# Performance work log

Hardware: AMD Instinct MI355X
Metric: run time of the kernel (lower is better)

Reference implementation:

```python
import jax, jax.numpy as jnp
import numpy as np


def setup_inputs() -> dict:
    key = jax.random.key(0)
    ks = jax.random.split(key, 7)
    BSZ, L, V, D = 4096, 50, 100000, 256
    acts_request = jax.random.randint(ks[0], (BSZ, L), 0, V, dtype=jnp.int32)
    acts_slot = jax.random.randint(ks[1], (BSZ, L), 0, V, dtype=jnp.int32)
    acts_value = jax.random.randint(ks[2], (BSZ, L), 0, V, dtype=jnp.int32)
    slot_names = jax.random.randint(ks[3], (BSZ, 4), 0, V, dtype=jnp.int32)
    ontology_emb = jax.random.normal(ks[4], (V, D), dtype=jnp.float32)
    # torch.nn.init.uniform(-0.01, 0.01)
    w1 = jax.random.uniform(ks[5], (D, D), dtype=jnp.float32, minval=-0.01, maxval=0.01)
    w2 = jax.random.uniform(ks[6], (D, D), dtype=jnp.float32, minval=-0.01, maxval=0.01)
    return {"acts_request": acts_request, "acts_slot": acts_slot,
            "acts_value": acts_value, "slot_names": slot_names,
            "ontology_emb": ontology_emb, "w1": w1, "w2": w2}


def reference(acts_request, acts_slot, acts_value, slot_names, ontology_emb, w1, w2):
    # ragged embedding gather + sum over the act lists -> (bsz, d)
    t_q = ontology_emb[acts_request].sum(axis=1)
    t_s = ontology_emb[acts_slot].sum(axis=1)
    t_v = ontology_emb[acts_value].sum(axis=1)
    c_s = ontology_emb[slot_names]                      # (bsz, 4, d)
    # matmul(w1, t_q) per batch: (bsz, d)
    g_q = jnp.einsum('ij,bj->bi', w1, t_q)
    g_sv = jnp.einsum('ij,bj->bi', w2, t_s + t_v)
    gates = (c_s
             + jax.nn.sigmoid(c_s * g_q[:, None, :])
             + jax.nn.sigmoid(c_s * g_sv[:, None, :]))
    return gates  # (bsz, 4, d)
```

## Files before the change

### kernel.cpp

```cpp
#include <hip/hip_runtime.h>

#define BLK     256
#define TBATCH  4
#define LLEN    50
#define DIM     256
#define DIM4    64

__device__ __forceinline__ float sigmoidf_(float x) {
    return 1.0f / (1.0f + __expf(-x));
}

__global__ __launch_bounds__(256) void transpose_w(
    const float* __restrict__ w1, const float* __restrict__ w2,
    float* __restrict__ wt1, float* __restrict__ wt2)
{
    __shared__ float tile[64][65];
    const int m  = blockIdx.x >> 4;
    const int t  = blockIdx.x & 15;
    const int ti = (t >> 2) * 64;
    const int tj = (t & 3) * 64;
    const float* src = m ? w2  : w1;
    float*       dst = m ? wt2 : wt1;
    const int tx = threadIdx.x & 63;
    const int ty = threadIdx.x >> 6;
    #pragma unroll
    for (int r = 0; r < 64; r += 4) {
        const int row = r + ty;
        tile[row][tx] = src[(ti + row) * DIM + tj + tx];
    }
    __syncthreads();
    #pragma unroll
    for (int r = 0; r < 64; r += 4) {
        const int row = r + ty;
        dst[(tj + row) * DIM + ti + tx] = tile[tx][row];
    }
}

__global__ __launch_bounds__(BLK, 4) void slotgate_fused(
    const int* __restrict__ acts_request,
    const int* __restrict__ acts_slot,
    const int* __restrict__ acts_value,
    const int* __restrict__ slot_names,
    const float* __restrict__ emb,
    const float* __restrict__ wt1,
    const float* __restrict__ wt2,
    float* __restrict__ out)
{
    __shared__ int    lds_iq[TBATCH * LLEN];
    __shared__ int    lds_is[TBATCH * LLEN];
    __shared__ int    lds_iv[TBATCH * LLEN];
    __shared__ float4 lds_tq [TBATCH * DIM4];
    __shared__ float4 lds_tsv[TBATCH * DIM4];
    __shared__ float  lds_gq [TBATCH * DIM];
    __shared__ float  lds_gsv[TBATCH * DIM];

    const int tid  = threadIdx.x;
    const int b0   = blockIdx.x * TBATCH;
    const int wv   = tid >> 6;
    const int lane = tid & 63;

    for (int t = tid; t < TBATCH * LLEN; t += BLK) {
        lds_iq[t] = acts_request[b0 * LLEN + t];
        lds_is[t] = acts_slot   [b0 * LLEN + t];
        lds_iv[t] = acts_value  [b0 * LLEN + t];
    }
    __syncthreads();

    const float4* emb4 = (const float4*)emb;

    {
        float4 aq  = make_float4(0.f, 0.f, 0.f, 0.f);
        float4 asv = make_float4(0.f, 0.f, 0.f, 0.f);
        const int* iqp = &lds_iq[wv * LLEN];
        const int* isp = &lds_is[wv * LLEN];
        const int* ivp = &lds_iv[wv * LLEN];
        #pragma unroll 5
        for (int l = 0; l < LLEN; l++) {
            float4 vq = emb4[iqp[l] * DIM4 + lane];
            float4 vs = emb4[isp[l] * DIM4 + lane];
            float4 vv = emb4[ivp[l] * DIM4 + lane];
            aq.x  += vq.x;        aq.y  += vq.y;        aq.z  += vq.z;        aq.w  += vq.w;
            asv.x += vs.x + vv.x; asv.y += vs.y + vv.y; asv.z += vs.z + vv.z; asv.w += vs.w + vv.w;
        }
        lds_tq [wv * DIM4 + lane] = aq;
        lds_tsv[wv * DIM4 + lane] = asv;
    }
    __syncthreads();

    {
        const int i = wv * 64 + lane;
        float accq [TBATCH] = {};
        float accsv[TBATCH] = {};
        for (int j4 = 0; j4 < DIM4; j4++) {
            float tqa[TBATCH][4], tsa[TBATCH][4];
            #pragma unroll
            for (int r = 0; r < TBATCH; r++) {
                float4 v = lds_tq [r * DIM4 + j4];
                tqa[r][0] = v.x; tqa[r][1] = v.y; tqa[r][2] = v.z; tqa[r][3] = v.w;
                float4 u = lds_tsv[r * DIM4 + j4];
                tsa[r][0] = u.x; tsa[r][1] = u.y; tsa[r][2] = u.z; tsa[r][3] = u.w;
            }
            #pragma unroll
            for (int k = 0; k < 4; k++) {
                const int j = j4 * 4 + k;
                const float w1v = wt1[j * DIM + i];
                const float w2v = wt2[j * DIM + i];
                #pragma unroll
                for (int r = 0; r < TBATCH; r++) {
                    accq [r] += w1v * tqa[r][k];
                    accsv[r] += w2v * tsa[r][k];
                }
            }
        }
        #pragma unroll
        for (int r = 0; r < TBATCH; r++) {
            lds_gq [r * DIM + i] = accq [r];
            lds_gsv[r * DIM + i] = accsv[r];
        }
    }
    __syncthreads();

    {
        const int tb   = tid >> 6;
        const int tcol = tid & 63;
        const int b    = b0 + tb;
        const float4* gq4 = (const float4*)lds_gq;
        const float4* gs4 = (const float4*)lds_gsv;
        const float4 gq = gq4[tb * DIM4 + tcol];
        const float4 gs = gs4[tb * DIM4 + tcol];
        float4* out4 = (float4*)out;
        #pragma unroll
        for (int s = 0; s < 4; s++) {
            const int slot = slot_names[b * 4 + s];
            float4 cs = emb4[slot * DIM4 + tcol];
            float4 g;
            g.x = cs.x + sigmoidf_(cs.x * gq.x) + sigmoidf_(cs.x * gs.x);
            g.y = cs.y + sigmoidf_(cs.y * gq.y) + sigmoidf_(cs.y * gs.y);
            g.z = cs.z + sigmoidf_(cs.z * gq.z) + sigmoidf_(cs.z * gs.z);
            g.w = cs.w + sigmoidf_(cs.w * gq.w) + sigmoidf_(cs.w * gs.w);
            out4[(b * 4 + s) * DIM4 + tcol] = g;
        }
    }
}

extern "C" void kernel_launch(void* const* d_in, const int* in_sizes, int n_in,
                              void* d_out, int out_size, void* d_ws, size_t ws_size,
                              hipStream_t stream) {
    const int*   acts_request = (const int*)  d_in[0];
    const int*   acts_slot    = (const int*)  d_in[1];
    const int*   acts_value   = (const int*)  d_in[2];
    const int*   slot_names   = (const int*)  d_in[3];
    const float* ontology_emb = (const float*)d_in[4];
    const float* w1           = (const float*)d_in[5];
    const float* w2           = (const float*)d_in[6];
    float*       out          = (float*)      d_out;

    float* wt1 = (float*)d_ws;
    float* wt2 = wt1 + DIM * DIM;

    const int bsz  = in_sizes[0] / LLEN;
    const int nblk = bsz / TBATCH;

    transpose_w<<<32, 256, 0, stream>>>(w1, w2, wt1, wt2);
    slotgate_fused<<<nblk, BLK, 0, stream>>>(
        acts_request, acts_slot, acts_value, slot_names,
        ontology_emb, wt1, wt2, out);
}
```

Baseline: 252.5 us.

## Double block size and split gather work across two waves per batch row

Raises the block to 512 threads so each batch row's 150 embedding lookups are split evenly between two wavefronts (75 each) instead of one wave doing all 150. The matvec stage is split so each thread computes two batch rows instead of four, and the epilogue loops over output elements. The aim is more memory-level parallelism and shorter per-wave gather chains on the latency-bound embedding gathers. In exchange, the larger block has to fit the new occupancy bound with fewer registers per thread, and the weight matrices are read twice per block.

```diff
diff --git a/kernel.cpp b/kernel.cpp
--- a/kernel.cpp
+++ b/kernel.cpp
@@ -1,8 +1,10 @@
 #include <hip/hip_runtime.h>
 
-#define BLK     256
+#define BLK     512
 #define TBATCH  4
 #define LLEN    50
+#define CONCAT  150
+#define CPAD    152
 #define DIM     256
 #define DIM4    64
 
@@ -36,7 +38,7 @@
     }
 }
 
-__global__ __launch_bounds__(BLK, 4) void slotgate_fused(
+__global__ __launch_bounds__(BLK, 8) void slotgate_fused(
     const int* __restrict__ acts_request,
     const int* __restrict__ acts_slot,
     const int* __restrict__ acts_value,
@@ -46,59 +48,85 @@
     const float* __restrict__ wt2,
     float* __restrict__ out)
 {
-    __shared__ int    lds_iq[TBATCH * LLEN];
-    __shared__ int    lds_is[TBATCH * LLEN];
-    __shared__ int    lds_iv[TBATCH * LLEN];
-    __shared__ float4 lds_tq [TBATCH * DIM4];
-    __shared__ float4 lds_tsv[TBATCH * DIM4];
-    __shared__ float  lds_gq [TBATCH * DIM];
-    __shared__ float  lds_gsv[TBATCH * DIM];
+    __shared__ int    lds_idx [TBATCH * CPAD];
+    __shared__ float4 lds_tq  [TBATCH * DIM4];
+    __shared__ float4 lds_tsv0[TBATCH * DIM4];
+    __shared__ float4 lds_tsv1[TBATCH * DIM4];
+    __shared__ float  lds_gq  [TBATCH * DIM];
+    __shared__ float  lds_gsv [TBATCH * DIM];
 
     const int tid  = threadIdx.x;
     const int b0   = blockIdx.x * TBATCH;
     const int wv   = tid >> 6;
     const int lane = tid & 63;
 
-    for (int t = tid; t < TBATCH * LLEN; t += BLK) {
-        lds_iq[t] = acts_request[b0 * LLEN + t];
-        lds_is[t] = acts_slot   [b0 * LLEN + t];
-        lds_iv[t] = acts_value  [b0 * LLEN + t];
+    for (int t = tid; t < TBATCH * CONCAT; t += BLK) {
+        const int row = t / CONCAT;
+        const int e   = t - row * CONCAT;
+        const int b   = b0 + row;
+        int idx;
+        if      (e < 50)  idx = acts_request[b * LLEN + e];
+        else if (e < 100) idx = acts_slot   [b * LLEN + e - 50];
+        else              idx = acts_value  [b * LLEN + e - 100];
+        lds_idx[row * CPAD + e] = idx;
     }
     __syncthreads();
 
     const float4* emb4 = (const float4*)emb;
 
     {
-        float4 aq  = make_float4(0.f, 0.f, 0.f, 0.f);
-        float4 asv = make_float4(0.f, 0.f, 0.f, 0.f);
-        const int* iqp = &lds_iq[wv * LLEN];
-        const int* isp = &lds_is[wv * LLEN];
-        const int* ivp = &lds_iv[wv * LLEN];
-        #pragma unroll 5
-        for (int l = 0; l < LLEN; l++) {
-            float4 vq = emb4[iqp[l] * DIM4 + lane];
-            float4 vs = emb4[isp[l] * DIM4 + lane];
-            float4 vv = emb4[ivp[l] * DIM4 + lane];
-            aq.x  += vq.x;        aq.y  += vq.y;        aq.z  += vq.z;        aq.w  += vq.w;
-            asv.x += vs.x + vv.x; asv.y += vs.y + vv.y; asv.z += vs.z + vv.z; asv.w += vs.w + vv.w;
+        const int grow = wv >> 1;
+        const int gh   = wv & 1;
+        const int* ip  = &lds_idx[grow * CPAD];
+        float4 accA = make_float4(0.f, 0.f, 0.f, 0.f);
+        float4 accB = make_float4(0.f, 0.f, 0.f, 0.f);
+        if (gh == 0) {
+            #pragma unroll 5
+            for (int e = 0; e < 50; e++) {
+                float4 v = emb4[ip[e] * DIM4 + lane];
+                accA.x += v.x; accA.y += v.y; accA.z += v.z; accA.w += v.w;
+            }
+            #pragma unroll 5
+            for (int e = 50; e < 75; e++) {
+                float4 v = emb4[ip[e] * DIM4 + lane];
+                accB.x += v.x; accB.y += v.y; accB.z += v.z; accB.w += v.w;
+            }
+            lds_tq  [grow * DIM4 + lane] = accA;
+            lds_tsv0[grow * DIM4 + lane] = accB;
+        } else {
+            #pragma unroll 5
+            for (int e = 75; e < 100; e++) {
+                float4 v = emb4[ip[e] * DIM4 + lane];
+                accA.x += v.x; accA.y += v.y; accA.z += v.z; accA.w += v.w;
+            }
+            #pragma unroll 5
+            for (int e = 100; e < 150; e++) {
+                float4 v = emb4[ip[e] * DIM4 + lane];
+                accB.x += v.x; accB.y += v.y; accB.z += v.z; accB.w += v.w;
+            }
+            float4 s;
+            s.x = accA.x + accB.x; s.y = accA.y + accB.y;
+            s.z = accA.z + accB.z; s.w = accA.w + accB.w;
+            lds_tsv1[grow * DIM4 + lane] = s;
         }
-        lds_tq [wv * DIM4 + lane] = aq;
-        lds_tsv[wv * DIM4 + lane] = asv;
     }
     __syncthreads();
 
     {
-        const int i = wv * 64 + lane;
-        float accq [TBATCH] = {};
-        float accsv[TBATCH] = {};
+        const int i  = tid & 255;
+        const int r0 = (tid >> 8) * 2;
+        float accq [2] = {};
+        float accsv[2] = {};
         for (int j4 = 0; j4 < DIM4; j4++) {
-            float tqa[TBATCH][4], tsa[TBATCH][4];
+            float tq[2][4], ts[2][4];
             #pragma unroll
-            for (int r = 0; r < TBATCH; r++) {
-                float4 v = lds_tq [r * DIM4 + j4];
-                tqa[r][0] = v.x; tqa[r][1] = v.y; tqa[r][2] = v.z; tqa[r][3] = v.w;
-                float4 u = lds_tsv[r * DIM4 + j4];
-                tsa[r][0] = u.x; tsa[r][1] = u.y; tsa[r][2] = u.z; tsa[r][3] = u.w;
+            for (int r = 0; r < 2; r++) {
+                float4 a = lds_tq  [(r0 + r) * DIM4 + j4];
+                float4 p = lds_tsv0[(r0 + r) * DIM4 + j4];
+                float4 q = lds_tsv1[(r0 + r) * DIM4 + j4];
+                tq[r][0] = a.x; tq[r][1] = a.y; tq[r][2] = a.z; tq[r][3] = a.w;
+                ts[r][0] = p.x + q.x; ts[r][1] = p.y + q.y;
+                ts[r][2] = p.z + q.z; ts[r][3] = p.w + q.w;
             }
             #pragma unroll
             for (int k = 0; k < 4; k++) {
@@ -106,39 +134,40 @@
                 const float w1v = wt1[j * DIM + i];
                 const float w2v = wt2[j * DIM + i];
                 #pragma unroll
-                for (int r = 0; r < TBATCH; r++) {
-                    accq [r] += w1v * tqa[r][k];
-                    accsv[r] += w2v * tsa[r][k];
+                for (int r = 0; r < 2; r++) {
+                    accq [r] += w1v * tq[r][k];
+                    accsv[r] += w2v * ts[r][k];
                 }
             }
         }
         #pragma unroll
-        for (int r = 0; r < TBATCH; r++) {
-            lds_gq [r * DIM + i] = accq [r];
-            lds_gsv[r * DIM + i] = accsv[r];
+        for (int r = 0; r < 2; r++) {
+            lds_gq [(r0 + r) * DIM + i] = accq [r];
+            lds_gsv[(r0 + r) * DIM + i] = accsv[r];
         }
     }
     __syncthreads();
 
     {
-        const int tb   = tid >> 6;
-        const int tcol = tid & 63;
-        const int b    = b0 + tb;
         const float4* gq4 = (const float4*)lds_gq;
         const float4* gs4 = (const float4*)lds_gsv;
-        const float4 gq = gq4[tb * DIM4 + tcol];
-        const float4 gs = gs4[tb * DIM4 + tcol];
         float4* out4 = (float4*)out;
         #pragma unroll
-        for (int s = 0; s < 4; s++) {
+        for (int t = tid; t < TBATCH * 4 * DIM4; t += BLK) {
+            const int row = t >> 8;
+            const int s   = (t >> 6) & 3;
+            const int col = t & 63;
+            const int b   = b0 + row;
             const int slot = slot_names[b * 4 + s];
-            float4 cs = emb4[slot * DIM4 + tcol];
+            float4 cs = emb4[slot * DIM4 + col];
+            float4 gq = gq4[row * DIM4 + col];
+            float4 gs = gs4[row * DIM4 + col];
             float4 g;
             g.x = cs.x + sigmoidf_(cs.x * gq.x) + sigmoidf_(cs.x * gs.x);
             g.y = cs.y + sigmoidf_(cs.y * gq.y) + sigmoidf_(cs.y * gs.y);
             g.z = cs.z + sigmoidf_(cs.z * gq.z) + sigmoidf_(cs.z * gs.z);
             g.w = cs.w + sigmoidf_(cs.w * gq.w) + sigmoidf_(cs.w * gs.w);
-            out4[(b * 4 + s) * DIM4 + tcol] = g;
+            out4[(b * 4 + s) * DIM4 + col] = g;
         }
     }
 }
```

Measured after the change: 257.2 us. Within noise of the previous version (+1.9%).
